# Performance work log

Hardware: AMD Instinct MI355X
Metric: run time of the kernel (lower is better)

The kernel has to match this reference:

```python
import jax, jax.numpy as jnp
import numpy as np
from jax import lax

KH, KW = 3, 3
K = KH * KW
STRIDE, PAD, DIL = 1, 1, 1
CIN, COUT = 64, 64


def setup_inputs() -> dict:
    key = jax.random.key(0)
    k1, k2, k3, k4 = jax.random.split(key, 4)
    B, H, W = 8, 96, 96
    x = jax.random.normal(k1, (B, CIN, H, W), dtype=jnp.float32)
    # offset/mask conv params (small so sampled offsets stay near the grid)
    w_off = jax.random.normal(k2, (3 * K, CIN, KH, KW), dtype=jnp.float32) * 0.01
    b_off = jnp.zeros((3 * K,), dtype=jnp.float32)
    # main deformable conv weight, uniform(-stdv, stdv) like reset_parameters
    stdv = 1.0 / np.sqrt(CIN * KH * KW)
    weight = jax.random.uniform(k3, (COUT, CIN, KH, KW), dtype=jnp.float32,
                                minval=-stdv, maxval=stdv)
    bias = jax.random.normal(k4, (COUT,), dtype=jnp.float32) * 0.01
    return {"x": x, "w_off": w_off, "b_off": b_off, "weight": weight, "bias": bias}


def _bilinear_sample(img, ys, xs):
    # img: [C,H,W]; ys, xs: [K,Ho,Wo] float sample coords. Zero outside borders.
    C, H, W = img.shape
    y0 = jnp.floor(ys)
    x0 = jnp.floor(xs)
    wy1 = ys - y0  # weight for y0+1
    wx1 = xs - x0
    wy0 = 1.0 - wy1
    wx0 = 1.0 - wx1

    def gather(yi, xi):
        yc = jnp.clip(yi, 0, H - 1).astype(jnp.int32)
        xc = jnp.clip(xi, 0, W - 1).astype(jnp.int32)
        valid = ((yi >= 0) & (yi <= H - 1) & (xi >= 0) & (xi <= W - 1))
        # [C,K,Ho,Wo]
        return img[:, yc, xc] * valid.astype(img.dtype)[None]

    return (gather(y0, x0) * (wy0 * wx0)[None]
            + gather(y0, x0 + 1) * (wy0 * wx1)[None]
            + gather(y0 + 1, x0) * (wy1 * wx0)[None]
            + gather(y0 + 1, x0 + 1) * (wy1 * wx1)[None])


def reference(x, w_off, b_off, weight, bias):
    B, C, H, W = x.shape
    # offset/mask conv (same geometry as main conv)
    om = lax.conv_general_dilated(
        x, w_off, window_strides=(STRIDE, STRIDE),
        padding=[(PAD, PAD), (PAD, PAD)], rhs_dilation=(DIL, DIL),
        dimension_numbers=("NCHW", "OIHW", "NCHW")) + b_off[None, :, None, None]
    Ho, Wo = om.shape[2], om.shape[3]
    offset = om[:, :2 * K].reshape(B, K, 2, Ho, Wo)  # interleaved (dy,dx) per tap
    dy, dx = offset[:, :, 0], offset[:, :, 1]         # [B,K,Ho,Wo]
    mask = jax.nn.sigmoid(om[:, 2 * K:])              # [B,K,Ho,Wo]

    k = jnp.arange(K)
    ky = (k // KW).astype(jnp.float32) * DIL  # [K]
    kx = (k % KW).astype(jnp.float32) * DIL
    oy = jnp.arange(Ho, dtype=jnp.float32) * STRIDE - PAD  # [Ho]
    ox = jnp.arange(Wo, dtype=jnp.float32) * STRIDE - PAD  # [Wo]
    ys = oy[None, None, :, None] + ky[None, :, None, None] + dy  # [B,K,Ho,Wo]
    xs = ox[None, None, None, :] + kx[None, :, None, None] + dx

    sampled = jax.vmap(_bilinear_sample)(x, ys, xs)  # [B,C,K,Ho,Wo]
    w_r = weight.reshape(weight.shape[0], C, K)      # [O,C,K]
    out = jnp.einsum("bkhw,bckhw,ock->bohw", mask, sampled, w_r)
    return out + bias[None, :, None, None]
```

## Files before the change

### kernel.cpp

```cpp
#include <hip/hip_runtime.h>
#include <math.h>

typedef __bf16 b16x8 __attribute__((ext_vector_type(8)));
typedef float  f32x4 __attribute__((ext_vector_type(4)));

#define B_    8
#define CIN_  64
#define COUT_ 64
#define Hs    96
#define Ws    96
#define PLANE (Hs*Ws)
#define IMG   (CIN_*PLANE)
#define NP    (B_*PLANE)
#define NBLK  (NP/32)

#define WR 7
#define WC 40
#define WPIX (WR*WC)
#define WBYTES (WPIX*128)

__device__ __forceinline__ int swz(int bid) { return (bid & 7) * (NBLK / 8) + (bid >> 3); }

__global__ void prep_xpose(const float* __restrict__ x,
                           const float* __restrict__ weight, const float* __restrict__ w_off,
                           __bf16* __restrict__ xT,
                           __bf16* __restrict__ wAB, __bf16* __restrict__ wAO) {
    int bid = blockIdx.x;
    if (bid < 288) {
        int p = bid * 256 + threadIdx.x;
        int b = p / PLANE, r = p - b * PLANE;
        const float* src = x + b * IMG + r;
        __bf16 buf[64];
#pragma unroll
        for (int c = 0; c < 64; ++c) buf[c] = (__bf16)src[c * PLANE];
        b16x8* dst = (b16x8*)(xT + (size_t)p * 64);
#pragma unroll
        for (int j = 0; j < 8; ++j) dst[j] = ((const b16x8*)buf)[j];
    } else {
        int i = (bid - 288) * 256 + threadIdx.x;
        if (i < 36864) {
            int e = i & 7, lane = (i >> 3) & 63, mt = (i >> 9) & 3, ks = (i >> 11) & 1, k = i >> 12;
            int o = mt * 16 + (lane & 15);
            int c = ks * 32 + ((lane >> 4) << 3) + e;
            wAB[i] = (__bf16)weight[o * 576 + c * 9 + k];
        }
        if (i < 18432) {
            int e = i & 7, lane = (i >> 3) & 63, mt = (i >> 9) & 1, ks = (i >> 10) & 1, t = i >> 11;
            int ch = mt * 16 + (lane & 15);
            int c  = ks * 32 + ((lane >> 4) << 3) + e;
            wAO[i] = (ch < 27) ? (__bf16)w_off[ch * 576 + c * 9 + t] : (__bf16)(0.f);
        }
    }
}

__global__ __launch_bounds__(256, 3)
void deform_mfma(const __bf16* __restrict__ xT,
                 const __bf16* __restrict__ wAO,
                 const float* __restrict__ b_off,
                 const __bf16* __restrict__ wAB,
                 const float* __restrict__ bias,
                 float* __restrict__ out) {
    __shared__ __align__(16) unsigned char smemWin[WBYTES];
    __shared__ float omP[2][2][28][16];

    int tid  = threadIdx.x;
    int lane = tid & 63;
    int g    = __builtin_amdgcn_readfirstlane(tid >> 6);
    int s    = g & 1;
    int kh   = g >> 1;
    int n    = lane & 15;
    int q    = lane >> 4;

    int pg0  = swz(blockIdx.x) * 32;
    int b    = pg0 / PLANE;
    int rblk = pg0 - b * PLANE;
    int h0   = rblk / Ws;
    int c0   = rblk - h0 * Ws;
    int w    = c0 + s * 16 + n;
    const __bf16* xTimg = xT + (size_t)b * PLANE * 64;
    const __bf16* xTb   = xTimg + kh * 32 + q * 8;

    const b16x8* wAOv = (const b16x8*)wAO;
    const b16x8* wABv = (const b16x8*)wAB;
    int boff = kh * 64 + q * 16;

#define LDSRD(sl) (*(const b16x8*)(smemWin + (sl) * 128 + (boff ^ (((sl) & 7) << 4))))

#pragma unroll
    for (int r2 = 0; r2 < 9; ++r2) {
        int idx = tid + r2 * 256;
        if (r2 < 8 || tid < (WPIX * 8 - 2048)) {
            int pix = idx >> 3, j = idx & 7;
            int yw = pix / WC, xw = pix - yw * WC;
            int ys = min(max(h0 - 3 + yw, 0), Hs - 1);
            int xs = min(max(c0 - 3 + xw, 0), Ws - 1);
            b16x8 v = *(const b16x8*)(xTimg + ((ys * Ws + xs) * 64) + j * 8);
            *(b16x8*)(smemWin + pix * 128 + ((j * 16) ^ ((pix & 7) << 4))) = v;
        }
    }
    __syncthreads();

    f32x4 accA0 = {0.f, 0.f, 0.f, 0.f};
    f32x4 accA1 = {0.f, 0.f, 0.f, 0.f};
    const b16x8 ZER = {};

#pragma unroll 3
    for (int t = 0; t < 9; ++t) {
        int ky = t / 3, kx = t - ky * 3;
        int yy = h0 - 1 + ky, xx = w - 1 + kx;
        bool mk = (yy >= 0 && yy < Hs && xx >= 0 && xx < Ws);
        int sl = (ky + 2) * WC + (s * 16 + n + kx + 2);
        b16x8 bf = LDSRD(sl);
        bf = mk ? bf : ZER;
        b16x8 af0 = wAOv[((t * 2 + kh) * 2 + 0) * 64 + lane];
        b16x8 af1 = wAOv[((t * 2 + kh) * 2 + 1) * 64 + lane];
        accA0 = __builtin_amdgcn_mfma_f32_16x16x32_bf16(af0, bf, accA0, 0, 0, 0);
        accA1 = __builtin_amdgcn_mfma_f32_16x16x32_bf16(af1, bf, accA1, 0, 0, 0);
    }
#pragma unroll
    for (int rg = 0; rg < 4; ++rg) {
        int ch = q * 4 + rg;
        omP[s][kh][ch][n] = accA0[rg] + (kh ? 0.f : b_off[ch]);
    }
#pragma unroll
    for (int rg = 0; rg < 4; ++rg) {
        int ch = 16 + q * 4 + rg;
        if (ch < 27) omP[s][kh][ch][n] = accA1[rg] + (kh ? 0.f : b_off[ch]);
    }
    __syncthreads();

    f32x4 acc0 = {0.f, 0.f, 0.f, 0.f};
    f32x4 acc1 = {0.f, 0.f, 0.f, 0.f};
    f32x4 acc2 = {0.f, 0.f, 0.f, 0.f};
    f32x4 acc3 = {0.f, 0.f, 0.f, 0.f};

    const float* om0 = &omP[s][0][0][0];
    const float* om1 = &omP[s][1][0][0];

#pragma unroll 3
    for (int k = 0; k < 9; ++k) {
        float dy = om0[(2 * k) * 16 + n]     + om1[(2 * k) * 16 + n];
        float dx = om0[(2 * k + 1) * 16 + n] + om1[(2 * k + 1) * 16 + n];
        float mo = om0[(18 + k) * 16 + n]    + om1[(18 + k) * 16 + n];

        b16x8 a0 = wABv[(k * 8 + kh * 4 + 0) * 64 + lane];
        b16x8 a1 = wABv[(k * 8 + kh * 4 + 1) * 64 + lane];
        b16x8 a2 = wABv[(k * 8 + kh * 4 + 2) * 64 + lane];
        b16x8 a3 = wABv[(k * 8 + kh * 4 + 3) * 64 + lane];

        float m  = 1.f / (1.f + __expf(-mo));
        int ky = k / 3, kx = k - ky * 3;
        float ysf = (float)(h0 - 1 + ky) + dy;
        float xsf = (float)(w  - 1 + kx) + dx;
        float y0f = floorf(ysf), x0f = floorf(xsf);
        float ly = ysf - y0f, lx = xsf - x0f;
        float hy = 1.f - ly, hx = 1.f - lx;
        int y0 = (int)y0f, x0 = (int)x0f, y1 = y0 + 1, x1 = x0 + 1;
        bool vy0 = (y0 >= 0) && (y0 < Hs), vy1 = (y1 >= 0) && (y1 < Hs);
        bool vx0 = (x0 >= 0) && (x0 < Ws), vx1 = (x1 >= 0) && (x1 < Ws);
        float W00 = (vy0 && vx0) ? m * hy * hx : 0.f;
        float W01 = (vy0 && vx1) ? m * hy * lx : 0.f;
        float W10 = (vy1 && vx0) ? m * ly * hx : 0.f;
        float W11 = (vy1 && vx1) ? m * ly * lx : 0.f;

        bool inw = (y0 >= h0 - 3) && (y1 <= h0 + 3) && (x0 >= c0 - 3) && (x1 <= c0 + 36);

        b16x8 e00, e01, e10, e11;
        if (inw) {
            int sl = (y0 - (h0 - 3)) * WC + (x0 - (c0 - 3));
            e00 = LDSRD(sl);
            e01 = LDSRD(sl + 1);
            e10 = LDSRD(sl + WC);
            e11 = LDSRD(sl + WC + 1);
        } else {
            int y0c = min(max(y0, 0), Hs - 1), y1c = min(max(y1, 0), Hs - 1);
            int x0c = min(max(x0, 0), Ws - 1), x1c = min(max(x1, 0), Ws - 1);
            e00 = *(const b16x8*)(xTb + (y0c * Ws + x0c) * 64);
            e01 = *(const b16x8*)(xTb + (y0c * Ws + x1c) * 64);
            e10 = *(const b16x8*)(xTb + (y1c * Ws + x0c) * 64);
            e11 = *(const b16x8*)(xTb + (y1c * Ws + x1c) * 64);
        }

        b16x8 fe;
#pragma unroll
        for (int j = 0; j < 8; ++j)
            fe[j] = (__bf16)((float)e00[j] * W00 + (float)e01[j] * W01 +
                             (float)e10[j] * W10 + (float)e11[j] * W11);

        acc0 = __builtin_amdgcn_mfma_f32_16x16x32_bf16(a0, fe, acc0, 0, 0, 0);
        acc1 = __builtin_amdgcn_mfma_f32_16x16x32_bf16(a1, fe, acc1, 0, 0, 0);
        acc2 = __builtin_amdgcn_mfma_f32_16x16x32_bf16(a2, fe, acc2, 0, 0, 0);
        acc3 = __builtin_amdgcn_mfma_f32_16x16x32_bf16(a3, fe, acc3, 0, 0, 0);
    }
#undef LDSRD

    __syncthreads();
    float* xch = (float*)smemWin;
    {
        f32x4* xw = (f32x4*)&xch[((s * 2 + kh) * 64 + lane) * 8];
        if (kh == 0) { xw[0] = acc2; xw[1] = acc3; }
        else         { xw[0] = acc0; xw[1] = acc1; }
    }
    __syncthreads();
    {
        const f32x4* xr = (const f32x4*)&xch[((s * 2 + (kh ^ 1)) * 64 + lane) * 8];
        f32x4 t0 = xr[0], t1 = xr[1];
        int rr = rblk + s * 16 + n;
        int ob = b * (COUT_ * PLANE) + rr;
        if (kh == 0) {
            f32x4 bs0 = *(const f32x4*)&bias[q * 4];
            f32x4 bs1 = *(const f32x4*)&bias[16 + q * 4];
#pragma unroll
            for (int rg = 0; rg < 4; ++rg) { int o =      q * 4 + rg; out[ob + o * PLANE] = acc0[rg] + t0[rg] + bs0[rg]; }
#pragma unroll
            for (int rg = 0; rg < 4; ++rg) { int o = 16 + q * 4 + rg; out[ob + o * PLANE] = acc1[rg] + t1[rg] + bs1[rg]; }
        } else {
            f32x4 bs2 = *(const f32x4*)&bias[32 + q * 4];
            f32x4 bs3 = *(const f32x4*)&bias[48 + q * 4];
#pragma unroll
            for (int rg = 0; rg < 4; ++rg) { int o = 32 + q * 4 + rg; out[ob + o * PLANE] = acc2[rg] + t0[rg] + bs2[rg]; }
#pragma unroll
            for (int rg = 0; rg < 4; ++rg) { int o = 48 + q * 4 + rg; out[ob + o * PLANE] = acc3[rg] + t1[rg] + bs3[rg]; }
        }
    }
}

extern "C" void kernel_launch(void* const* d_in, const int* in_sizes, int n_in,
                              void* d_out, int out_size, void* d_ws, size_t ws_size,
                              hipStream_t stream) {
    const float* x      = (const float*)d_in[0];
    const float* w_off  = (const float*)d_in[1];
    const float* b_off  = (const float*)d_in[2];
    const float* weight = (const float*)d_in[3];
    const float* bias   = (const float*)d_in[4];
    float* out = (float*)d_out;

    char* ws = (char*)d_ws;
    __bf16* wAB = (__bf16*)ws;
    __bf16* wAO = (__bf16*)(ws + 73728);
    __bf16* xT  = (__bf16*)(ws + 131072);

    prep_xpose<<<432, 256, 0, stream>>>(x, weight, w_off, xT, wAB, wAO);
    deform_mfma<<<NBLK, 256, 0, stream>>>(xT, wAO, b_off, wAB, bias, out);
}
```

Before: 118.1 us.

## Tile blocks as 2x16 pixel patches with smaller halo window

Changes each block's 32-pixel tile from a 1x32 row strip to a 2-row by 16-column patch. The LDS halo window shrinks from 7x40 to 8x24 pixels, so each block loads fewer halo bytes and uses less shared memory. Launch bounds are raised to allow 4 blocks per SM. The trade-off is that narrower columns shorten each coalesced row segment, and the higher occupancy target may force register spills.

New measurement: 115.1 us. 1.03x faster.

```diff
diff --git a/kernel.cpp b/kernel.cpp
--- a/kernel.cpp
+++ b/kernel.cpp
@@ -14,8 +14,8 @@
 #define NP    (B_*PLANE)
 #define NBLK  (NP/32)
 
-#define WR 7
-#define WC 40
+#define WR 8
+#define WC 24
 #define WPIX (WR*WC)
 #define WBYTES (WPIX*128)
 
@@ -53,7 +53,7 @@
     }
 }
 
-__global__ __launch_bounds__(256, 3)
+__global__ __launch_bounds__(256, 4)
 void deform_mfma(const __bf16* __restrict__ xT,
                  const __bf16* __restrict__ wAO,
                  const float* __restrict__ b_off,
@@ -71,12 +71,16 @@
     int n    = lane & 15;
     int q    = lane >> 4;
 
-    int pg0  = swz(blockIdx.x) * 32;
-    int b    = pg0 / PLANE;
-    int rblk = pg0 - b * PLANE;
-    int h0   = rblk / Ws;
-    int c0   = rblk - h0 * Ws;
-    int w    = c0 + s * 16 + n;
+    int t    = swz(blockIdx.x);
+    int b    = t / 288;
+    int rem  = t - b * 288;
+    int rp   = rem / 6;
+    int ct   = rem - rp * 6;
+    int h0   = rp * 2;
+    int c0   = ct * 16;
+    int hrow = h0 + s;
+    int w    = c0 + n;
+
     const __bf16* xTimg = xT + (size_t)b * PLANE * 64;
     const __bf16* xTb   = xTimg + kh * 32 + q * 8;
 
@@ -87,16 +91,14 @@
 #define LDSRD(sl) (*(const b16x8*)(smemWin + (sl) * 128 + (boff ^ (((sl) & 7) << 4))))
 
 #pragma unroll
-    for (int r2 = 0; r2 < 9; ++r2) {
+    for (int r2 = 0; r2 < 6; ++r2) {
         int idx = tid + r2 * 256;
-        if (r2 < 8 || tid < (WPIX * 8 - 2048)) {
-            int pix = idx >> 3, j = idx & 7;
-            int yw = pix / WC, xw = pix - yw * WC;
-            int ys = min(max(h0 - 3 + yw, 0), Hs - 1);
-            int xs = min(max(c0 - 3 + xw, 0), Ws - 1);
-            b16x8 v = *(const b16x8*)(xTimg + ((ys * Ws + xs) * 64) + j * 8);
-            *(b16x8*)(smemWin + pix * 128 + ((j * 16) ^ ((pix & 7) << 4))) = v;
-        }
+        int pix = idx >> 3, j = idx & 7;
+        int yw = pix / WC, xw = pix - yw * WC;
+        int ys = min(max(h0 - 3 + yw, 0), Hs - 1);
+        int xs = min(max(c0 - 3 + xw, 0), Ws - 1);
+        b16x8 v = *(const b16x8*)(xTimg + ((ys * Ws + xs) * 64) + j * 8);
+        *(b16x8*)(smemWin + pix * 128 + ((j * 16) ^ ((pix & 7) << 4))) = v;
     }
     __syncthreads();
 
@@ -105,15 +107,15 @@
     const b16x8 ZER = {};
 
 #pragma unroll 3
-    for (int t = 0; t < 9; ++t) {
-        int ky = t / 3, kx = t - ky * 3;
-        int yy = h0 - 1 + ky, xx = w - 1 + kx;
+    for (int tt = 0; tt < 9; ++tt) {
+        int ky = tt / 3, kx = tt - ky * 3;
+        int yy = hrow - 1 + ky, xx = w - 1 + kx;
         bool mk = (yy >= 0 && yy < Hs && xx >= 0 && xx < Ws);
-        int sl = (ky + 2) * WC + (s * 16 + n + kx + 2);
+        int sl = (s + 2 + ky) * WC + (n + 2 + kx);
         b16x8 bf = LDSRD(sl);
         bf = mk ? bf : ZER;
-        b16x8 af0 = wAOv[((t * 2 + kh) * 2 + 0) * 64 + lane];
-        b16x8 af1 = wAOv[((t * 2 + kh) * 2 + 1) * 64 + lane];
+        b16x8 af0 = wAOv[((tt * 2 + kh) * 2 + 0) * 64 + lane];
+        b16x8 af1 = wAOv[((tt * 2 + kh) * 2 + 1) * 64 + lane];
         accA0 = __builtin_amdgcn_mfma_f32_16x16x32_bf16(af0, bf, accA0, 0, 0, 0);
         accA1 = __builtin_amdgcn_mfma_f32_16x16x32_bf16(af1, bf, accA1, 0, 0, 0);
     }
@@ -150,8 +152,8 @@
 
         float m  = 1.f / (1.f + __expf(-mo));
         int ky = k / 3, kx = k - ky * 3;
-        float ysf = (float)(h0 - 1 + ky) + dy;
-        float xsf = (float)(w  - 1 + kx) + dx;
+        float ysf = (float)(hrow - 1 + ky) + dy;
+        float xsf = (float)(w    - 1 + kx) + dx;
         float y0f = floorf(ysf), x0f = floorf(xsf);
         float ly = ysf - y0f, lx = xsf - x0f;
         float hy = 1.f - ly, hx = 1.f - lx;
@@ -163,7 +165,7 @@
         float W10 = (vy1 && vx0) ? m * ly * hx : 0.f;
         float W11 = (vy1 && vx1) ? m * ly * lx : 0.f;
 
-        bool inw = (y0 >= h0 - 3) && (y1 <= h0 + 3) && (x0 >= c0 - 3) && (x1 <= c0 + 36);
+        bool inw = (y0 >= h0 - 3) && (y1 <= h0 + 4) && (x0 >= c0 - 3) && (x1 <= c0 + 20);
 
         b16x8 e00, e01, e10, e11;
         if (inw) {
@@ -205,7 +207,7 @@
     {
         const f32x4* xr = (const f32x4*)&xch[((s * 2 + (kh ^ 1)) * 64 + lane) * 8];
         f32x4 t0 = xr[0], t1 = xr[1];
-        int rr = rblk + s * 16 + n;
+        int rr = hrow * Ws + w;
         int ob = b * (COUT_ * PLANE) + rr;
         if (kh == 0) {
             f32x4 bs0 = *(const f32x4*)&bias[q * 4];
```
